# Kernel tuning notes

Measured on AMD Instinct MI355X. Metric: run time of the kernel, lower is better.

Reference implementation:

```python
import jax, jax.numpy as jnp
import numpy as np

B, C, H, W, D = 2, 512, 16, 16, 16
GROUPS = 32
EPS = 1e-6


def setup_inputs() -> dict:
    key = jax.random.key(0)
    ks = jax.random.split(key, 6)
    s = 1.0 / np.sqrt(C)
    inp = {
        "x": jax.random.normal(ks[0], (B, C, H, W, D), jnp.float32),
        "gn_w": jnp.ones((C,), jnp.float32),
        "gn_b": jnp.zeros((C,), jnp.float32),
        "wq": jax.random.normal(ks[1], (C, C), jnp.float32) * s,
        "bq": jnp.zeros((C,), jnp.float32),
        "wk": jax.random.normal(ks[2], (C, C), jnp.float32) * s,
        "bk": jnp.zeros((C,), jnp.float32),
        "wv": jax.random.normal(ks[3], (C, C), jnp.float32) * s,
        "bv": jnp.zeros((C,), jnp.float32),
        "wp": jax.random.normal(ks[4], (C, C), jnp.float32) * s,
        "bp": jnp.zeros((C,), jnp.float32),
    }
    return inp


def reference(x, gn_w, gn_b, wq, bq, wk, bk, wv, bv, wp, bp):
    b, c, h, w, d = x.shape
    # GroupNorm(32 groups, eps=1e-6, affine)
    xg = x.reshape(b, GROUPS, c // GROUPS, h, w, d)
    mu = xg.mean(axis=(2, 3, 4, 5), keepdims=True)
    var = xg.var(axis=(2, 3, 4, 5), keepdims=True)
    hn = ((xg - mu) / jnp.sqrt(var + EPS)).reshape(b, c, h, w, d)
    hn = hn * gn_w[None, :, None, None, None] + gn_b[None, :, None, None, None]
    # 1x1x1 conv projections == per-token channel matmul
    n = h * w * d
    hf = hn.reshape(b, c, n)
    q = jnp.einsum('oc,bcn->bon', wq, hf) + bq[None, :, None]  # [b,c,n]
    k = jnp.einsum('oc,bcn->bon', wk, hf) + bk[None, :, None]
    v = jnp.einsum('oc,bcn->bon', wv, hf) + bv[None, :, None]
    # attention: scores[b,i,j] = sum_c q[b,c,i] k[b,c,j] / sqrt(c)
    scores = jnp.einsum('bci,bcj->bij', q, k) * (c ** -0.5)
    attn = jax.nn.softmax(scores, axis=2)  # [b,n,n]
    # out[b,c,i] = sum_j v[b,c,j] attn[b,i,j]
    o = jnp.einsum('bij,bcj->bci', attn, v)
    o = jnp.einsum('oc,bcn->bon', wp, o) + bp[None, :, None]
    return x + o.reshape(b, c, h, w, d)
```

## Files before the change

kernel.cpp:

```cpp
#include <hip/hip_runtime.h>
#include <hip/hip_bf16.h>
#include <stdint.h>

typedef short short8 __attribute__((ext_vector_type(8)));
typedef float f32x4  __attribute__((ext_vector_type(4)));
typedef float f32x2  __attribute__((ext_vector_type(2)));
typedef float f32x16 __attribute__((ext_vector_type(16)));
typedef int   i32x4  __attribute__((ext_vector_type(4)));
typedef int   i32x8  __attribute__((ext_vector_type(8)));
typedef unsigned char uchar;

#define B_ 2
#define C_ 512
#define N_ 4096
#define G_ 32
#define WN (C_ * C_)
#define PREP_BLOCKS 4101

static __device__ __forceinline__ short f2bf(float f) {
    return __builtin_bit_cast(short, __float2bfloat16(f));
}
static __device__ __forceinline__ uchar f2fp8(float f) {
    return (uchar)(__builtin_amdgcn_cvt_pk_fp8_f32(f, f, 0, false) & 0xff);
}

static __device__ __forceinline__ void async16(uchar* lds_wave_base, const uchar* g) {
    auto l  = (__attribute__((address_space(3))) unsigned int*)(uintptr_t)(lds_wave_base);
    auto gg = (const __attribute__((address_space(1))) unsigned int*)(g);
    __builtin_amdgcn_global_load_lds(gg, l, 16, 0, 0);
}

__global__ void prep_stats(const float* __restrict__ wq, const float* __restrict__ wk,
                           const float* __restrict__ wv, const float* __restrict__ wp,
                           const float* __restrict__ bq, const float* __restrict__ bk,
                           const float* __restrict__ x,
                           uchar* __restrict__ Wb, float* __restrict__ bqk,
                           float* __restrict__ raw) {
    if (blockIdx.x < PREP_BLOCKS) {
        int i = blockIdx.x * 256 + threadIdx.x;
        if (i < 4 * WN) {
            const float* src = (i < 2*WN) ? ((i < WN) ? wq : wk) : ((i < 3*WN) ? wv : wp);
            Wb[i] = f2fp8(src[i & (WN - 1)] * 16.f);
        } else if (i < 4*WN + 1024) {
            int j = i - 4*WN;
            bqk[j] = (j < C_) ? bq[j] : bk[j - C_];
        }
        return;
    }
    const int idx = blockIdx.x - PREP_BLOCKS;
    const int bg = idx >> 2, qt = idx & 3;
    const float4* p = (const float4*)(x + (size_t)bg * 16 * N_ + (size_t)qt * 4 * N_);
    int tid = threadIdx.x;
    float s = 0.f, sq = 0.f;
    #pragma unroll
    for (int rep = 0; rep < 16; rep++) {
        float4 t = p[rep * 256 + tid];
        s  += t.x + t.y + t.z + t.w;
        sq += t.x*t.x + t.y*t.y + t.z*t.z + t.w*t.w;
    }
    __shared__ float rs[256], rq[256];
    rs[tid] = s; rq[tid] = sq;
    __syncthreads();
    for (int h = 128; h > 0; h >>= 1) {
        if (tid < h) { rs[tid] += rs[tid+h]; rq[tid] += rq[tid+h]; }
        __syncthreads();
    }
    if (tid == 0) {
        raw[idx*2+0] = rs[0];
        raw[idx*2+1] = rq[0];
    }
}

__global__ void gn_apply(const float* __restrict__ x, const float* __restrict__ raw,
                         const float* __restrict__ gw, const float* __restrict__ gb,
                         uchar* __restrict__ hn) {
    __shared__ uchar t[64 * 68];
    const int n0 = blockIdx.x * 64, c0 = blockIdx.y * 64, b = blockIdx.z;
    const int lane = threadIdx.x & 63, w = threadIdx.x >> 6;
    const float inv = 1.f / (16.f * N_);
    #pragma unroll
    for (int rep = 0; rep < 16; rep++) {
        int c  = rep * 4 + w;
        int cc = c0 + c;
        int g  = cc >> 4;
        int base = (b*G_ + g) * 8;
        float mean = (raw[base] + raw[base+2] + raw[base+4] + raw[base+6]) * inv;
        float var  = (raw[base+1] + raw[base+3] + raw[base+5] + raw[base+7]) * inv - mean * mean;
        float rstd = rsqrtf(var + 1e-6f);
        float sc = gw[cc] * rstd;
        float bi = gb[cc] - mean * sc;
        float v = x[((size_t)(b*C_ + cc)) * N_ + n0 + lane];
        t[lane*68 + c] = f2fp8(v * sc + bi);
    }
    __syncthreads();
    #pragma unroll
    for (int rep = 0; rep < 16; rep++) {
        int n = rep * 4 + w;
        hn[((size_t)(b*N_ + n0 + n)) * C_ + c0 + lane] = t[n*68 + lane];
    }
}

template<int BM, int BN, int BIAS_MODE, int OUT_MODE, int K, int SWZ>
__global__ __launch_bounds__(256, ((BM + BN) <= 256) ? 3 : 2)
void gemm_nt8(const uchar* __restrict__ A, int lda, long long sAz,
              const uchar* __restrict__ Bm, int ldb, long long sBz,
              void* __restrict__ Cv, int ldc, long long sCz,
              const float* __restrict__ bias,
              const float* __restrict__ res,
              float alpha) {
    constexpr int MI = BM / 64;
    constexpr int NI = BN / 64;
    constexpr int AC = BM / 64;
    constexpr int BC = BN / 64;
    constexpr int T  = K / 64;
    constexpr int D  = (BM + BN) / 64;
    constexpr unsigned WAITD = 0xF70u | D;
    constexpr unsigned WAIT0 = 0xF70u;
    __shared__ uchar As[3][BM * 64];
    __shared__ uchar Bs[3][BN * 64];

    int bx, by, bz;
    if (SWZ == 1) {
        int fid = blockIdx.x;
        int xcd = fid & 7, j = fid >> 3;
        int gg = (j >> 1) * 8 + xcd;
        bx = j & 1; by = gg & 63; bz = gg >> 6;
    } else if (SWZ == 2) {
        int fid = blockIdx.x;
        int xcd = fid & 7, j = fid >> 3;
        bz = j >> 6;
        int r = j & 63;
        by = (xcd << 2) | (r >> 4);
        bx = r & 15;
    } else { bx = blockIdx.x; by = blockIdx.y; bz = blockIdx.z; }

    const int tid  = threadIdx.x;
    const int lane = tid & 63;
    const int wid  = tid >> 6;
    const int wr   = wid >> 1;
    const int wc   = wid & 1;
    const int m0 = by * BM;
    const int n0 = bx * BN;

    const int r  = tid >> 2;
    const int gc = (tid & 3) ^ ((r >> 1) & 3);
    const uchar* Ap = A  + sAz * bz + (size_t)(m0 + r) * lda + gc * 16;
    const uchar* Bp = Bm + sBz * bz + (size_t)(n0 + r) * ldb + gc * 16;

    f32x16 acc[MI][NI];
    #pragma unroll
    for (int i = 0; i < MI; i++)
        #pragma unroll
        for (int j = 0; j < NI; j++)
            #pragma unroll
            for (int e = 0; e < 16; e++)
                acc[i][j][e] = 0.f;

    const int rl = lane & 31;
    const int hk = (lane >> 5) * 2;

    #define ISSUE(IB, u) do { size_t _kb = (size_t)(u) * 64; \
        _Pragma("unroll") \
        for (int c = 0; c < AC; c++) \
            async16(&As[IB][c * 4096 + wid * 1024], Ap + (size_t)c * 64 * lda + _kb); \
        _Pragma("unroll") \
        for (int c = 0; c < BC; c++) \
            async16(&Bs[IB][c * 4096 + wid * 1024], Bp + (size_t)c * 64 * ldb + _kb); } while (0)

    #define STEP(Bf, DO_ISSUE, IB, u, DO_BAR, WIMM) do { \
        i32x8 af[MI], bf[NI]; \
        _Pragma("unroll") \
        for (int i = 0; i < MI; i++) { \
            int ar = wr*(BM/2) + i*32 + rl; \
            int ao = ar*64 + ((hk ^ ((ar>>1)&3)) << 4); \
            *(i32x4*)&af[i]       = *(const i32x4*)&As[Bf][ao]; \
            *(((i32x4*)&af[i])+1) = *(const i32x4*)&As[Bf][ao ^ 16]; \
        } \
        _Pragma("unroll") \
        for (int i = 0; i < NI; i++) { \
            int br = wc*(BN/2) + i*32 + rl; \
            int bo = br*64 + ((hk ^ ((br>>1)&3)) << 4); \
            *(i32x4*)&bf[i]       = *(const i32x4*)&Bs[Bf][bo]; \
            *(((i32x4*)&bf[i])+1) = *(const i32x4*)&Bs[Bf][bo ^ 16]; \
        } \
        if (DO_ISSUE) ISSUE(IB, u); \
        _Pragma("unroll") \
        for (int mi = 0; mi < MI; mi++) \
            _Pragma("unroll") \
            for (int ni = 0; ni < NI; ni++) \
                acc[mi][ni] = __builtin_amdgcn_mfma_scale_f32_32x32x64_f8f6f4( \
                    af[mi], bf[ni], acc[mi][ni], 0, 0, 0, 127, 0, 127); \
        if (DO_BAR) { __builtin_amdgcn_s_waitcnt(WIMM); __builtin_amdgcn_s_barrier(); } \
    } while (0)

    ISSUE(0, 0);
    ISSUE(1, 1);
    __builtin_amdgcn_s_waitcnt(WAITD);
    __builtin_amdgcn_s_barrier();

    constexpr int Gm = (T - 2) / 3;
    for (int m = 0; m < Gm; m++) {
        STEP(0, 1, 2, m*3 + 2, 1, WAITD);
        STEP(1, 1, 0, m*3 + 3, 1, WAITD);
        STEP(2, 1, 1, m*3 + 4, 1, WAITD);
    }
    if (T - 3*Gm == 2) {
        STEP(0, 0, 0, 0, 1, WAIT0);
        STEP(1, 0, 0, 0, 0, 0);
    } else {
        STEP(0, 1, 2, T-2, 1, WAITD);
        STEP(1, 1, 0, T-1, 1, WAITD);
        STEP(2, 0, 0, 0, 1, WAIT0);
        STEP(0, 0, 0, 0, 0, 0);
    }
    #undef ISSUE
    #undef STEP

    const int rh = (lane >> 5) * 4;
    #pragma unroll
    for (int mi = 0; mi < MI; mi++) {
        #pragma unroll
        for (int ni = 0; ni < NI; ni++) {
            int cc = n0 + wc*(BN/2) + ni*32 + rl;
            float cb = (BIAS_MODE == 1) ? bias[cc] : 0.f;
            #pragma unroll
            for (int g = 0; g < 4; g++) {
                #pragma unroll
                for (int r4 = 0; r4 < 4; r4++) {
                    int rr = m0 + wr*(BM/2) + mi*32 + g*8 + rh + r4;
                    float val = acc[mi][ni][g*4 + r4] * alpha + cb;
                    if (BIAS_MODE == 2) val += bias[rr];
                    long long idx = sCz * bz + (long long)rr * ldc + cc;
                    if (OUT_MODE == 0)      ((short*)Cv)[idx] = f2bf(val);
                    else if (OUT_MODE == 2) ((float*)Cv)[idx] = val + res[idx];
                    else                    ((uchar*)Cv)[idx] = f2fp8(val);
                }
            }
        }
    }
}

__global__ void softmax_rows8(uchar* __restrict__ S) {
    const int lane = threadIdx.x & 63;
    const int wave = threadIdx.x >> 6;
    const size_t row = (size_t)blockIdx.x * 4 + wave;
    uint4* rp = (uint4*)(S + row * N_);
    uint4 d[4];
    float f[64];
    float mx = -3.0e38f;
    #pragma unroll
    for (int c = 0; c < 4; c++) {
        d[c] = rp[c * 64 + lane];
        unsigned wv[4] = {d[c].x, d[c].y, d[c].z, d[c].w};
        #pragma unroll
        for (int u = 0; u < 4; u++) {
            f32x2 lo = __builtin_amdgcn_cvt_pk_f32_fp8(wv[u], false);
            f32x2 hi = __builtin_amdgcn_cvt_pk_f32_fp8(wv[u], true);
            int b = c*16 + u*4;
            f[b+0] = lo[0]; f[b+1] = lo[1]; f[b+2] = hi[0]; f[b+3] = hi[1];
            mx = fmaxf(mx, fmaxf(fmaxf(lo[0], lo[1]), fmaxf(hi[0], hi[1])));
        }
    }
    #pragma unroll
    for (int off = 32; off > 0; off >>= 1)
        mx = fmaxf(mx, __shfl_xor(mx, off));
    float sum = 0.f;
    const float k = 0.0625f;
    #pragma unroll
    for (int j = 0; j < 64; j++) { f[j] = __expf((f[j] - mx) * k); sum += f[j]; }
    #pragma unroll
    for (int off = 32; off > 0; off >>= 1)
        sum += __shfl_xor(sum, off);
    float inv = 256.f / sum;
    #pragma unroll
    for (int c = 0; c < 4; c++) {
        unsigned wv[4];
        #pragma unroll
        for (int u = 0; u < 4; u++) {
            int b = c*16 + u*4;
            int o = 0;
            o = __builtin_amdgcn_cvt_pk_fp8_f32(f[b+0]*inv, f[b+1]*inv, o, false);
            o = __builtin_amdgcn_cvt_pk_fp8_f32(f[b+2]*inv, f[b+3]*inv, o, true);
            wv[u] = (unsigned)o;
        }
        uint4 ov; ov.x = wv[0]; ov.y = wv[1]; ov.z = wv[2]; ov.w = wv[3];
        rp[c * 64 + lane] = ov;
    }
}

extern "C" void kernel_launch(void* const* d_in, const int* in_sizes, int n_in,
                              void* d_out, int out_size, void* d_ws, size_t ws_size,
                              hipStream_t stream) {
    const float* x   = (const float*)d_in[0];
    const float* gnw = (const float*)d_in[1];
    const float* gnb = (const float*)d_in[2];
    const float* wq  = (const float*)d_in[3];
    const float* bq  = (const float*)d_in[4];
    const float* wk  = (const float*)d_in[5];
    const float* bk  = (const float*)d_in[6];
    const float* wv  = (const float*)d_in[7];
    const float* bv  = (const float*)d_in[8];
    const float* wp  = (const float*)d_in[9];
    const float* bp  = (const float*)d_in[10];
    float* out = (float*)d_out;
    char*  ws  = (char*)d_ws;

    float* raw = (float*)(ws + 0);
    float* bqk = (float*)(ws + 8192);
    uchar* Wb  = (uchar*)(ws + 65536);
    uchar* Hn  = (uchar*)(ws + (2ull  << 20));
    uchar* QK8 = (uchar*)(ws + (8ull  << 20));
    uchar* V8  = (uchar*)(ws + (16ull << 20));
    uchar* Ot8 = (uchar*)(ws + (20ull << 20));
    uchar* Sb  = (uchar*)(ws + (24ull << 20));

    prep_stats<<<PREP_BLOCKS + 256, 256, 0, stream>>>(wq, wk, wv, wp, bq, bk, x, Wb, bqk, raw);
    gn_apply<<<dim3(N_/64, C_/64, B_), 256, 0, stream>>>(x, raw, gnw, gnb, Hn);

    const long long sHn = (long long)N_ * C_;
    const long long sQK = (long long)N_ * 1024;
    const long long sV  = (long long)C_ * N_;
    const long long sS  = (long long)N_ * N_;

    gemm_nt8<128,128,1,3,512,0><<<dim3(8, 32, 2), 256, 0, stream>>>(
        Hn, C_, sHn, Wb, C_, 0, QK8, 1024, sQK, bqk, nullptr, 1.f/16.f);
    gemm_nt8<64,256,2,3,512,0><<<dim3(16, 8, 2), 256, 0, stream>>>(
        Wb + 2*WN, C_, 0, Hn, C_, sHn, V8, N_, sV, bv, nullptr, 1.f/16.f);

    const float alphaS = 0.044194173824159216f * 16.f;
    gemm_nt8<128,256,0,3,512,2><<<1024, 256, 0, stream>>>(
        QK8, 1024, sQK, QK8 + 512, 1024, sQK, Sb, N_, sS, nullptr, nullptr, alphaS);
    softmax_rows8<<<B_*N_/4, 256, 0, stream>>>(Sb);
    gemm_nt8<64,256,0,3,4096,1><<<256, 256, 0, stream>>>(
        Sb, N_, sS, V8, N_, sV, Ot8, C_, sHn, nullptr, nullptr, 1.f/16.f);
    gemm_nt8<64,256,2,2,512,0><<<dim3(16, 8, 2), 256, 0, stream>>>(
        Wb + 3*WN, C_, 0, Ot8, C_, sHn, out, N_, (long long)C_*N_, bp, x, 1.f/256.f);
}
```

Before: 189.9 us.

## Fuse V projection into QK GEMM, vectorize weight prep, shrink attention GEMM tiles

The V projection is folded into the Q/K projection GEMM by extending the N dimension to 1536. Columns at or beyond 1024 are written transposed into V8 as packed fp8x4 stores, which removes one launch and a second pass over Hn. Weight conversion now reads float4 and packs four fp8 values per store, so it needs far fewer blocks. The score, PV and output GEMMs move to narrower 128-wide tiles with twice as many blocks and updated swizzles, trading some operand reuse for more parallelism and occupancy.

Result: slower. 215.2 us (+13.4%).

```diff
diff --git a/kernel.cpp b/kernel.cpp
--- a/kernel.cpp
+++ b/kernel.cpp
@@ -15,13 +15,19 @@
 #define N_ 4096
 #define G_ 32
 #define WN (C_ * C_)
-#define PREP_BLOCKS 4101
+#define PREP_W 1024
+#define PREP_BLOCKS 1030
 
 static __device__ __forceinline__ short f2bf(float f) {
     return __builtin_bit_cast(short, __float2bfloat16(f));
 }
 static __device__ __forceinline__ uchar f2fp8(float f) {
     return (uchar)(__builtin_amdgcn_cvt_pk_fp8_f32(f, f, 0, false) & 0xff);
+}
+static __device__ __forceinline__ unsigned pk4fp8(float a, float b, float c, float d) {
+    int w = __builtin_amdgcn_cvt_pk_fp8_f32(a, b, 0, false);
+    w = __builtin_amdgcn_cvt_pk_fp8_f32(c, d, w, true);
+    return (unsigned)w;
 }
 
 static __device__ __forceinline__ void async16(uchar* lds_wave_base, const uchar* g) {
@@ -33,18 +39,23 @@
 __global__ void prep_stats(const float* __restrict__ wq, const float* __restrict__ wk,
                            const float* __restrict__ wv, const float* __restrict__ wp,
                            const float* __restrict__ bq, const float* __restrict__ bk,
+                           const float* __restrict__ bv,
                            const float* __restrict__ x,
-                           uchar* __restrict__ Wb, float* __restrict__ bqk,
+                           uchar* __restrict__ Wb, float* __restrict__ bqkv,
                            float* __restrict__ raw) {
+    if (blockIdx.x < PREP_W) {
+        int i4 = blockIdx.x * 256 + threadIdx.x;
+        int base = i4 * 4;
+        int wsel = base >> 18;
+        const float* src = (wsel == 0) ? wq : (wsel == 1) ? wk : (wsel == 2) ? wv : wp;
+        float4 t = *(const float4*)(src + (base & (WN - 1)));
+        ((unsigned*)Wb)[i4] = pk4fp8(t.x*16.f, t.y*16.f, t.z*16.f, t.w*16.f);
+        return;
+    }
     if (blockIdx.x < PREP_BLOCKS) {
-        int i = blockIdx.x * 256 + threadIdx.x;
-        if (i < 4 * WN) {
-            const float* src = (i < 2*WN) ? ((i < WN) ? wq : wk) : ((i < 3*WN) ? wv : wp);
-            Wb[i] = f2fp8(src[i & (WN - 1)] * 16.f);
-        } else if (i < 4*WN + 1024) {
-            int j = i - 4*WN;
-            bqk[j] = (j < C_) ? bq[j] : bk[j - C_];
-        }
+        int j = (blockIdx.x - PREP_W) * 256 + threadIdx.x;
+        if (j < 1536)
+            bqkv[j] = (j < C_) ? bq[j] : (j < 2*C_) ? bk[j - C_] : bv[j - 2*C_];
         return;
     }
     const int idx = blockIdx.x - PREP_BLOCKS;
@@ -106,7 +117,7 @@
               const uchar* __restrict__ Bm, int ldb, long long sBz,
               void* __restrict__ Cv, int ldc, long long sCz,
               const float* __restrict__ bias,
-              const float* __restrict__ res,
+              const void* __restrict__ resv,
               float alpha) {
     constexpr int MI = BM / 64;
     constexpr int NI = BN / 64;
@@ -123,15 +134,15 @@
     if (SWZ == 1) {
         int fid = blockIdx.x;
         int xcd = fid & 7, j = fid >> 3;
-        int gg = (j >> 1) * 8 + xcd;
-        bx = j & 1; by = gg & 63; bz = gg >> 6;
+        int gg = (j >> 2) * 8 + xcd;
+        bx = j & 3; by = gg & 63; bz = gg >> 6;
     } else if (SWZ == 2) {
         int fid = blockIdx.x;
         int xcd = fid & 7, j = fid >> 3;
-        bz = j >> 6;
-        int r = j & 63;
-        by = (xcd << 2) | (r >> 4);
-        bx = r & 15;
+        bz = j >> 7;
+        int r = j & 127;
+        by = (xcd << 2) | (r >> 5);
+        bx = r & 31;
     } else { bx = blockIdx.x; by = blockIdx.y; bz = blockIdx.z; }
 
     const int tid  = threadIdx.x;
@@ -225,6 +236,17 @@
             float cb = (BIAS_MODE == 1) ? bias[cc] : 0.f;
             #pragma unroll
             for (int g = 0; g < 4; g++) {
+                if (OUT_MODE == 4 && n0 >= 1024) {
+                    int rr0 = m0 + wr*(BM/2) + mi*32 + g*8 + rh;
+                    float v0 = acc[mi][ni][g*4+0] * alpha + cb;
+                    float v1 = acc[mi][ni][g*4+1] * alpha + cb;
+                    float v2 = acc[mi][ni][g*4+2] * alpha + cb;
+                    float v3 = acc[mi][ni][g*4+3] * alpha + cb;
+                    uchar* V8 = (uchar*)(uintptr_t)resv;
+                    *(unsigned*)(V8 + (long long)C_*N_*bz + (size_t)(cc - 1024) * N_ + rr0)
+                        = pk4fp8(v0, v1, v2, v3);
+                    continue;
+                }
                 #pragma unroll
                 for (int r4 = 0; r4 < 4; r4++) {
                     int rr = m0 + wr*(BM/2) + mi*32 + g*8 + rh + r4;
@@ -232,7 +254,7 @@
                     if (BIAS_MODE == 2) val += bias[rr];
                     long long idx = sCz * bz + (long long)rr * ldc + cc;
                     if (OUT_MODE == 0)      ((short*)Cv)[idx] = f2bf(val);
-                    else if (OUT_MODE == 2) ((float*)Cv)[idx] = val + res[idx];
+                    else if (OUT_MODE == 2) ((float*)Cv)[idx] = val + ((const float*)resv)[idx];
                     else                    ((uchar*)Cv)[idx] = f2fp8(val);
                 }
             }
@@ -305,8 +327,8 @@
     float* out = (float*)d_out;
     char*  ws  = (char*)d_ws;
 
-    float* raw = (float*)(ws + 0);
-    float* bqk = (float*)(ws + 8192);
+    float* raw  = (float*)(ws + 0);
+    float* bqkv = (float*)(ws + 8192);
     uchar* Wb  = (uchar*)(ws + 65536);
     uchar* Hn  = (uchar*)(ws + (2ull  << 20));
     uchar* QK8 = (uchar*)(ws + (8ull  << 20));
@@ -314,7 +336,7 @@
     uchar* Ot8 = (uchar*)(ws + (20ull << 20));
     uchar* Sb  = (uchar*)(ws + (24ull << 20));
 
-    prep_stats<<<PREP_BLOCKS + 256, 256, 0, stream>>>(wq, wk, wv, wp, bq, bk, x, Wb, bqk, raw);
+    prep_stats<<<PREP_BLOCKS + 256, 256, 0, stream>>>(wq, wk, wv, wp, bq, bk, bv, x, Wb, bqkv, raw);
     gn_apply<<<dim3(N_/64, C_/64, B_), 256, 0, stream>>>(x, raw, gnw, gnb, Hn);
 
     const long long sHn = (long long)N_ * C_;
@@ -322,17 +344,15 @@
     const long long sV  = (long long)C_ * N_;
     const long long sS  = (long long)N_ * N_;
 
-    gemm_nt8<128,128,1,3,512,0><<<dim3(8, 32, 2), 256, 0, stream>>>(
-        Hn, C_, sHn, Wb, C_, 0, QK8, 1024, sQK, bqk, nullptr, 1.f/16.f);
-    gemm_nt8<64,256,2,3,512,0><<<dim3(16, 8, 2), 256, 0, stream>>>(
-        Wb + 2*WN, C_, 0, Hn, C_, sHn, V8, N_, sV, bv, nullptr, 1.f/16.f);
+    gemm_nt8<128,128,1,4,512,0><<<dim3(12, 32, 2), 256, 0, stream>>>(
+        Hn, C_, sHn, Wb, C_, 0, QK8, 1024, sQK, bqkv, V8, 1.f/16.f);
 
     const float alphaS = 0.044194173824159216f * 16.f;
-    gemm_nt8<128,256,0,3,512,2><<<1024, 256, 0, stream>>>(
+    gemm_nt8<128,128,0,3,512,2><<<2048, 256, 0, stream>>>(
         QK8, 1024, sQK, QK8 + 512, 1024, sQK, Sb, N_, sS, nullptr, nullptr, alphaS);
     softmax_rows8<<<B_*N_/4, 256, 0, stream>>>(Sb);
-    gemm_nt8<64,256,0,3,4096,1><<<256, 256, 0, stream>>>(
+    gemm_nt8<64,128,0,3,4096,1><<<512, 256, 0, stream>>>(
         Sb, N_, sS, V8, N_, sV, Ot8, C_, sHn, nullptr, nullptr, 1.f/16.f);
-    gemm_nt8<64,256,2,2,512,0><<<dim3(16, 8, 2), 256, 0, stream>>>(
+    gemm_nt8<64,128,2,2,512,0><<<dim3(32, 8, 2), 256, 0, stream>>>(
         Wb + 3*WN, C_, 0, Ot8, C_, sHn, out, N_, (long long)C_*N_, bp, x, 1.f/256.f);
 }
```
